# Optimization experiments

Hardware: AMD Instinct MI355X
Metric: run time of the kernel (lower is better)

The kernel has to match this reference:

```python
import jax, jax.numpy as jnp
import numpy as np
import math

B, S, D, H = 2, 2048, 1024, 16
HD = D // H  # head dim = 64


def setup_inputs() -> dict:
    key = jax.random.key(0)
    ks = jax.random.split(key, 8)
    scale = 1.0 / math.sqrt(D)
    return {
        "x": jax.random.normal(ks[0], (B, S, D), dtype=jnp.float32),
        "mask": jax.random.randint(ks[1], (B, S, S), 0, 2).astype(bool),
        "Wq": jax.random.normal(ks[2], (D, D), dtype=jnp.float32) * scale,
        "bq": jax.random.normal(ks[3], (D,), dtype=jnp.float32) * 0.01,
        "Wk": jax.random.normal(ks[4], (D, D), dtype=jnp.float32) * scale,
        "bk": jax.random.normal(ks[5], (D,), dtype=jnp.float32) * 0.01,
        "Wv": jax.random.normal(ks[6], (D, D), dtype=jnp.float32) * scale,
        "bv": jax.random.normal(ks[7], (D,), dtype=jnp.float32) * 0.01,
    }


def reference(x, mask, Wq, bq, Wk, bk, Wv, bv):
    # Linear projections (weights stored as [in, out])
    q = x @ Wq + bq  # [B,S,D]
    k = x @ Wk + bk
    v = x @ Wv + bv
    # split heads -> [B,H,S,HD]
    q = q.reshape(B, S, H, HD).transpose(0, 2, 1, 3)
    k = k.reshape(B, S, H, HD).transpose(0, 2, 1, 3)
    v = v.reshape(B, S, H, HD).transpose(0, 2, 1, 3)
    scores = jnp.einsum("bhqd,bhkd->bhqk", q, k) / jnp.sqrt(jnp.float32(HD))
    # Faithful to the source: masked_fill_(mask, -inf) is immediately
    # overwritten by masked_fill_(mask, 0), so masked positions end up 0
    # BEFORE the softmax (a quirk of the original module).
    scores = jnp.where(mask[:, None, :, :], 0.0, scores)
    attn = jax.nn.softmax(scores, axis=-1)  # dropout=0.0 (eval)
    out = jnp.einsum("bhqk,bhkd->bhqd", attn, v)
    return out.transpose(0, 2, 1, 3).reshape(B, S, D)
```

## Files before the change

### kernel.cpp

```cpp
#include <hip/hip_runtime.h>
#include <cstdint>
#include <cstddef>

static constexpr int B_ = 2, S_ = 2048, D_ = 1024, H_ = 16, HD_ = 64;

typedef float f32x4 __attribute__((ext_vector_type(4)));
typedef short bf16x8 __attribute__((ext_vector_type(8)));

__device__ __forceinline__ unsigned short f2bf(float f) {
    union { float f; unsigned int u; } v; v.f = f;
    unsigned int r = v.u + 0x7FFFu + ((v.u >> 16) & 1u);
    return (unsigned short)(r >> 16);
}

__device__ __forceinline__ unsigned pack2bf(float a, float b) {
#if __has_builtin(__builtin_amdgcn_cvt_pk_bf16_f32)
    auto p = __builtin_amdgcn_cvt_pk_bf16_f32(a, b);
    unsigned u; __builtin_memcpy(&u, &p, 4);
    return u;
#else
    return (unsigned)f2bf(a) | ((unsigned)f2bf(b) << 16);
#endif
}

__device__ __forceinline__ void gload_lds16(const void* g, void* l) {
    __builtin_amdgcn_global_load_lds(
        (const __attribute__((address_space(1))) void*)g,
        (__attribute__((address_space(3))) void*)l, 16, 0, 0);
}

__global__ __launch_bounds__(256)
void prep(const float* __restrict__ x, unsigned short* __restrict__ xo,
          const int* __restrict__ m, unsigned char* __restrict__ mo,
          const float* __restrict__ Wq, const float* __restrict__ Wk,
          const float* __restrict__ Wv, unsigned short* __restrict__ wt) {
    __shared__ unsigned short Ts[64][72];
    const int bid = blockIdx.x, t = threadIdx.x;
    if (bid < 2048) {
        size_t i = ((size_t)bid * 256 + t) * 8;
        float4 a = *(const float4*)(x + i);
        float4 c = *(const float4*)(x + i + 4);
        uint4 r;
        r.x = pack2bf(a.x, a.y); r.y = pack2bf(a.z, a.w);
        r.z = pack2bf(c.x, c.y); r.w = pack2bf(c.z, c.w);
        *(uint4*)(xo + i) = r;
    } else if (bid < 4096) {
        size_t i = ((size_t)(bid - 2048) * 256 + t) * 16;
        uint4 r;
        unsigned w[4];
        #pragma unroll
        for (int g = 0; g < 4; ++g) {
            int4 v = *(const int4*)(m + i + g * 4);
            w[g] = (v.x ? 1u : 0u) | (v.y ? 1u << 8 : 0u) |
                   (v.z ? 1u << 16 : 0u) | (v.w ? 1u << 24 : 0u);
        }
        r.x = w[0]; r.y = w[1]; r.z = w[2]; r.w = w[3];
        *(uint4*)(mo + i) = r;
    } else {
        const int tid = bid - 4096;
        const int mat = tid >> 8, tile = tid & 255;
        const float* __restrict__ W = (mat == 0) ? Wq : (mat == 1) ? Wk : Wv;
        unsigned short* __restrict__ o = wt + (size_t)mat * D_ * D_;
        const int n0 = (tile & 15) * 64, k0 = (tile >> 4) * 64;
        {
            const int nl = t & 63, kb = t >> 6;
            #pragma unroll
            for (int i = 0; i < 16; ++i) {
                int k = kb + i * 4;
                Ts[nl][k] = f2bf(W[(size_t)(k0 + k) * D_ + n0 + nl]);
            }
        }
        __syncthreads();
        {
            const int kl = t & 63, nb = t >> 6;
            #pragma unroll
            for (int i = 0; i < 16; ++i) {
                int n = nb + i * 4;
                o[(size_t)(n0 + n) * D_ + k0 + kl] = Ts[n][kl];
            }
        }
    }
}

__global__ __launch_bounds__(256)
void qkv_gemm(const unsigned short* __restrict__ xb, const unsigned short* __restrict__ wt,
              const float* __restrict__ bq, const float* __restrict__ bk,
              const float* __restrict__ bv,
              unsigned short* __restrict__ qo, unsigned short* __restrict__ ko,
              unsigned short* __restrict__ vto) {
    const int bx = blockIdx.x;
    const int by = blockIdx.y;
    const int mat = bx >> 3;
    const int ncol0 = (bx & 7) * 128;
    const float* __restrict__ bias = (mat == 0) ? bq : (mat == 1) ? bk : bv;
    const unsigned short* __restrict__ Wm = wt + (size_t)mat * D_ * D_;

    __shared__ unsigned short As[2][128 * 32];
    __shared__ unsigned short Bs[2][128 * 32];

    const int t = threadIdx.x;
    const int w = t >> 6, lane = t & 63;
    const int l15 = lane & 15, quad = lane >> 4;
    const int mw = (w >> 1) * 64, nw = (w & 1) * 64;
    const int rowBase = by * 128;

    const int r16 = lane >> 2;
    const int sslot = lane & 3;
    const int sg = (sslot ^ ((r16 >> 1) & 3)) * 8;
    const int rcol = (quad ^ ((l15 >> 1) & 3)) * 8;

    f32x4 acc[4][4] = {};

    #pragma unroll
    for (int j = 0; j < 2; ++j) {
        const int r0 = w * 32 + j * 16;
        gload_lds16(xb + (size_t)(rowBase + r0 + r16) * D_ + sg, &As[0][r0 * 32]);
        gload_lds16(Wm + (size_t)(ncol0 + r0 + r16) * D_ + sg, &Bs[0][r0 * 32]);
    }

    for (int it = 0; it < 32; ++it) {
        const int cur = it & 1;
        __syncthreads();
        if (it + 1 < 32) {
            const int ktn = (it + 1) * 32;
            #pragma unroll
            for (int j = 0; j < 2; ++j) {
                const int r0 = w * 32 + j * 16;
                gload_lds16(xb + (size_t)(rowBase + r0 + r16) * D_ + ktn + sg,
                            &As[cur ^ 1][r0 * 32]);
                gload_lds16(Wm + (size_t)(ncol0 + r0 + r16) * D_ + ktn + sg,
                            &Bs[cur ^ 1][r0 * 32]);
            }
        }

        bf16x8 a[4], b[4];
        #pragma unroll
        for (int i = 0; i < 4; ++i)
            a[i] = *(const bf16x8*)&As[cur][(mw + i * 16 + l15) * 32 + rcol];
        #pragma unroll
        for (int j = 0; j < 4; ++j)
            b[j] = *(const bf16x8*)&Bs[cur][(nw + j * 16 + l15) * 32 + rcol];
        #pragma unroll
        for (int i = 0; i < 4; ++i)
            #pragma unroll
            for (int j = 0; j < 4; ++j)
                acc[i][j] = __builtin_amdgcn_mfma_f32_16x16x32_bf16(a[i], b[j], acc[i][j], 0, 0, 0);
    }

    if (mat < 2) {
        unsigned short* __restrict__ O = (mat == 0) ? qo : ko;
        const float osc = (mat == 0) ? 0.18033688011112443f : 1.0f;
        #pragma unroll
        for (int j = 0; j < 4; ++j) {
            const int col = ncol0 + nw + j * 16 + l15;
            const float bb = bias[col];
            #pragma unroll
            for (int i = 0; i < 4; ++i)
                #pragma unroll
                for (int r = 0; r < 4; ++r) {
                    const int m = rowBase + mw + i * 16 + quad * 4 + r;
                    O[(size_t)m * D_ + col] = f2bf((acc[i][j][r] + bb) * osc);
                }
        }
    } else {
        #pragma unroll
        for (int j = 0; j < 4; ++j) {
            const int col = ncol0 + nw + j * 16 + l15;
            const float bb = bias[col];
            const int hh = col >> 6, hd = col & 63;
            #pragma unroll
            for (int i = 0; i < 4; ++i) {
                const int m0 = rowBase + mw + i * 16 + quad * 4;
                const int bg = m0 >> 11, s0 = m0 & 2047;
                ushort4 pk;
                pk.x = f2bf(acc[i][j][0] + bb);
                pk.y = f2bf(acc[i][j][1] + bb);
                pk.z = f2bf(acc[i][j][2] + bb);
                pk.w = f2bf(acc[i][j][3] + bb);
                *(ushort4*)&vto[(((size_t)bg * H_ + hh) * HD_ + hd) * S_ + s0] = pk;
            }
        }
    }
}

__global__ __launch_bounds__(256)
void attn_mfma(const unsigned short* __restrict__ qmat,
               const unsigned short* __restrict__ kmat,
               const unsigned short* __restrict__ vtg,
               const unsigned char* __restrict__ msk, float* __restrict__ out) {
    const int h = blockIdx.x, qt = blockIdx.y, b = blockIdx.z;
    const int t = threadIdx.x, w = t >> 6, lane = t & 63;
    const int l15 = lane & 15, quad = lane >> 4;
    const int q0 = qt * 128;

    __shared__ unsigned short Ks[2][64 * 64];
    __shared__ unsigned short Vs[2][64 * 64];
    __shared__ __align__(16) unsigned short Ps[128][72];

    const size_t bh = (size_t)b * S_ * D_ + (size_t)h * HD_;
    const unsigned short* __restrict__ qp = qmat + bh;
    const unsigned short* __restrict__ kp = kmat + bh;
    const unsigned short* __restrict__ vp = vtg + ((size_t)b * H_ + h) * HD_ * S_;
    const unsigned char* __restrict__ mb = msk + (size_t)b * S_ * S_;

    const int rs = lane >> 3, sslot = lane & 7;
    const int sg = (sslot ^ rs) * 8;

    bf16x8 qfr[2][2];
    #pragma unroll
    for (int nt = 0; nt < 2; ++nt)
        #pragma unroll
        for (int kst = 0; kst < 2; ++kst)
            qfr[nt][kst] = *(const bf16x8*)(qp +
                (size_t)(q0 + w * 32 + nt * 16 + l15) * D_ + kst * 32 + quad * 8);

    f32x4 accO[2][4] = {};
    f32x4 lsA[2] = {};
    bf16x8 ones;
    #pragma unroll
    for (int i = 0; i < 8; ++i) ones[i] = (short)0x3F80;

    #pragma unroll
    for (int j = 0; j < 2; ++j) {
        const int rb = w * 16 + j * 8;
        gload_lds16(kp + (size_t)(rb + rs) * D_ + sg, &Ks[0][rb * 64]);
        gload_lds16(vp + (size_t)(rb + rs) * S_ + sg, &Vs[0][rb * 64]);
    }

    for (int it = 0; it < 32; ++it) {
        const int cur = it & 1;
        const int kt = it * 64;
        __syncthreads();

        unsigned mu[2][4];
        #pragma unroll
        for (int nt = 0; nt < 2; ++nt) {
            const int qr = w * 32 + nt * 16 + l15;
            const unsigned char* __restrict__ mrow = mb + (size_t)(q0 + qr) * S_ + kt;
            #pragma unroll
            for (int mt = 0; mt < 4; ++mt)
                mu[nt][mt] = *(const unsigned*)(mrow + mt * 16 + quad * 4);
        }

        if (it + 1 < 32) {
            const int ktn = kt + 64;
            #pragma unroll
            for (int j = 0; j < 2; ++j) {
                const int rb = w * 16 + j * 8;
                gload_lds16(kp + (size_t)(ktn + rb + rs) * D_ + sg, &Ks[cur ^ 1][rb * 64]);
                gload_lds16(vp + (size_t)(rb + rs) * S_ + ktn + sg, &Vs[cur ^ 1][rb * 64]);
            }
        }

        f32x4 sc[4][2] = {};
        #pragma unroll
        for (int kst = 0; kst < 2; ++kst) {
            bf16x8 kfr[4];
            #pragma unroll
            for (int mt = 0; mt < 4; ++mt) {
                const int R = mt * 16 + l15;
                kfr[mt] = *(const bf16x8*)&Ks[cur][R * 64 + (((kst * 4 + quad) ^ (l15 & 7)) * 8)];
            }
            #pragma unroll
            for (int mt = 0; mt < 4; ++mt)
                #pragma unroll
                for (int nt = 0; nt < 2; ++nt)
                    sc[mt][nt] = __builtin_amdgcn_mfma_f32_16x16x32_bf16(kfr[mt], qfr[nt][kst], sc[mt][nt], 0, 0, 0);
        }

        #pragma unroll
        for (int nt = 0; nt < 2; ++nt) {
            const int qr = w * 32 + nt * 16 + l15;
            #pragma unroll
            for (int mt = 0; mt < 4; ++mt) {
                float p[4];
                #pragma unroll
                for (int r = 0; r < 4; ++r) {
                    float e = __builtin_amdgcn_exp2f(sc[mt][nt][r]);
                    p[r] = ((mu[nt][mt] >> (8 * r)) & 0xFFu) ? 1.0f : e;
                }
                uint2 pk;
                pk.x = pack2bf(p[0], p[1]);
                pk.y = pack2bf(p[2], p[3]);
                *(uint2*)&Ps[qr][mt * 16 + quad * 4] = pk;
            }
        }

        #pragma unroll
        for (int kst = 0; kst < 2; ++kst) {
            bf16x8 vfr[4];
            #pragma unroll
            for (int dt = 0; dt < 4; ++dt) {
                const int R = dt * 16 + l15;
                vfr[dt] = *(const bf16x8*)&Vs[cur][R * 64 + (((kst * 4 + quad) ^ (l15 & 7)) * 8)];
            }
            #pragma unroll
            for (int mt = 0; mt < 2; ++mt) {
                bf16x8 pfr = *(const bf16x8*)&Ps[w * 32 + mt * 16 + l15][kst * 32 + quad * 8];
                #pragma unroll
                for (int dt = 0; dt < 4; ++dt)
                    accO[mt][dt] = __builtin_amdgcn_mfma_f32_16x16x32_bf16(pfr, vfr[dt], accO[mt][dt], 0, 0, 0);
                lsA[mt] = __builtin_amdgcn_mfma_f32_16x16x32_bf16(pfr, ones, lsA[mt], 0, 0, 0);
            }
        }
    }

    float* __restrict__ ob = out + ((size_t)b * S_ + q0) * D_ + (size_t)h * HD_;
    #pragma unroll
    for (int mt = 0; mt < 2; ++mt)
        #pragma unroll
        for (int r = 0; r < 4; ++r) {
            const float inv = 1.0f / lsA[mt][r];
            const int qr = w * 32 + mt * 16 + quad * 4 + r;
            #pragma unroll
            for (int dt = 0; dt < 4; ++dt)
                ob[(size_t)qr * D_ + dt * 16 + l15] = accO[mt][dt][r] * inv;
        }
}

extern "C" void kernel_launch(void* const* d_in, const int* in_sizes, int n_in,
                              void* d_out, int out_size, void* d_ws, size_t ws_size,
                              hipStream_t stream) {
    (void)in_sizes; (void)n_in; (void)out_size; (void)ws_size;
    const float* x    = (const float*)d_in[0];
    const int*   mask = (const int*)d_in[1];
    const float* Wq   = (const float*)d_in[2];
    const float* bq   = (const float*)d_in[3];
    const float* Wk   = (const float*)d_in[4];
    const float* bk   = (const float*)d_in[5];
    const float* Wv   = (const float*)d_in[6];
    const float* bv   = (const float*)d_in[7];
    float* out = (float*)d_out;

    const size_t M1 = (size_t)1024 * 1024;
    unsigned short* xb  = (unsigned short*)d_ws;
    unsigned short* wtb = xb + 4 * M1;
    unsigned short* qb  = wtb + 3 * M1;
    unsigned short* kb  = qb + 4 * M1;
    unsigned short* vtb = kb + 4 * M1;
    unsigned char*  mk  = (unsigned char*)(vtb + 4 * M1);

    prep<<<4864, 256, 0, stream>>>(x, xb, mask, mk, Wq, Wk, Wv, wtb);
    qkv_gemm<<<dim3(24, 32), 256, 0, stream>>>(xb, wtb, bq, bk, bv, qb, kb, vtb);
    attn_mfma<<<dim3(16, 16, 2), 256, 0, stream>>>(qb, kb, vtb, mk, out);
}
```

Baseline: 234.7 us.

## Split attention over key halves with a combine pass, load V fragments from global

The attention kernel now splits the key range into two halves. This doubles the grid to 1024 blocks so more CUs are busy, and each half writes unnormalized partial outputs and row sums, with the first half's output stored in bf16. A new combine kernel adds the two partial outputs and normalizes by the summed row sums. V fragments are now read directly from global memory instead of being staged through LDS. The mask is stored inverted so that masking becomes a multiply by the mask byte before exp2, and the P tile in LDS gets an XOR swizzle. The trade-offs are an extra launch, extra traffic for the partial outputs, and some precision loss from the bf16 partial.

```diff
diff --git a/kernel.cpp b/kernel.cpp
--- a/kernel.cpp
+++ b/kernel.cpp
@@ -11,6 +11,10 @@
     union { float f; unsigned int u; } v; v.f = f;
     unsigned int r = v.u + 0x7FFFu + ((v.u >> 16) & 1u);
     return (unsigned short)(r >> 16);
+}
+__device__ __forceinline__ float bf2f(unsigned short h) {
+    union { unsigned int u; float f; } v; v.u = ((unsigned int)h) << 16;
+    return v.f;
 }
 
 __device__ __forceinline__ unsigned pack2bf(float a, float b) {
@@ -20,6 +24,19 @@
     return u;
 #else
     return (unsigned)f2bf(a) | ((unsigned)f2bf(b) << 16);
+#endif
+}
+
+__device__ __forceinline__ float ubyte2f(unsigned u, int r) {
+#if __has_builtin(__builtin_amdgcn_cvt_f32_ubyte0)
+    switch (r) {
+        case 0: return __builtin_amdgcn_cvt_f32_ubyte0(u);
+        case 1: return __builtin_amdgcn_cvt_f32_ubyte1(u);
+        case 2: return __builtin_amdgcn_cvt_f32_ubyte2(u);
+        default: return __builtin_amdgcn_cvt_f32_ubyte3(u);
+    }
+#else
+    return (float)((u >> (8 * r)) & 0xFFu);
 #endif
 }
 
@@ -51,8 +68,8 @@
         #pragma unroll
         for (int g = 0; g < 4; ++g) {
             int4 v = *(const int4*)(m + i + g * 4);
-            w[g] = (v.x ? 1u : 0u) | (v.y ? 1u << 8 : 0u) |
-                   (v.z ? 1u << 16 : 0u) | (v.w ? 1u << 24 : 0u);
+            w[g] = (v.x ? 0u : 1u) | (v.y ? 0u : 1u << 8) |
+                   (v.z ? 0u : 1u << 16) | (v.w ? 0u : 1u << 24);
         }
         r.x = w[0]; r.y = w[1]; r.z = w[2]; r.w = w[3];
         *(uint4*)(mo + i) = r;
@@ -187,15 +204,18 @@
 void attn_mfma(const unsigned short* __restrict__ qmat,
                const unsigned short* __restrict__ kmat,
                const unsigned short* __restrict__ vtg,
-               const unsigned char* __restrict__ msk, float* __restrict__ out) {
-    const int h = blockIdx.x, qt = blockIdx.y, b = blockIdx.z;
+               const unsigned char* __restrict__ msk,
+               unsigned short* __restrict__ O0, float* __restrict__ O1,
+               float* __restrict__ lws) {
+    const int qt = blockIdx.x, h = blockIdx.y;
+    const int b = blockIdx.z >> 1, half = blockIdx.z & 1;
     const int t = threadIdx.x, w = t >> 6, lane = t & 63;
     const int l15 = lane & 15, quad = lane >> 4;
     const int q0 = qt * 128;
+    const int kb0 = half * 1024;
 
     __shared__ unsigned short Ks[2][64 * 64];
-    __shared__ unsigned short Vs[2][64 * 64];
-    __shared__ __align__(16) unsigned short Ps[128][72];
+    __shared__ unsigned short Ps[128 * 64];
 
     const size_t bh = (size_t)b * S_ * D_ + (size_t)h * HD_;
     const unsigned short* __restrict__ qp = qmat + bh;
@@ -205,6 +225,7 @@
 
     const int rs = lane >> 3, sslot = lane & 7;
     const int sg = (sslot ^ rs) * 8;
+    const int l7 = l15 & 7;
 
     bf16x8 qfr[2][2];
     #pragma unroll
@@ -223,13 +244,12 @@
     #pragma unroll
     for (int j = 0; j < 2; ++j) {
         const int rb = w * 16 + j * 8;
-        gload_lds16(kp + (size_t)(rb + rs) * D_ + sg, &Ks[0][rb * 64]);
-        gload_lds16(vp + (size_t)(rb + rs) * S_ + sg, &Vs[0][rb * 64]);
-    }
-
-    for (int it = 0; it < 32; ++it) {
+        gload_lds16(kp + (size_t)(kb0 + rb + rs) * D_ + sg, &Ks[0][rb * 64]);
+    }
+
+    for (int it = 0; it < 16; ++it) {
         const int cur = it & 1;
-        const int kt = it * 64;
+        const int kt = kb0 + it * 64;
         __syncthreads();
 
         unsigned mu[2][4];
@@ -242,13 +262,12 @@
                 mu[nt][mt] = *(const unsigned*)(mrow + mt * 16 + quad * 4);
         }
 
-        if (it + 1 < 32) {
+        if (it + 1 < 16) {
             const int ktn = kt + 64;
             #pragma unroll
             for (int j = 0; j < 2; ++j) {
                 const int rb = w * 16 + j * 8;
                 gload_lds16(kp + (size_t)(ktn + rb + rs) * D_ + sg, &Ks[cur ^ 1][rb * 64]);
-                gload_lds16(vp + (size_t)(rb + rs) * S_ + ktn + sg, &Vs[cur ^ 1][rb * 64]);
             }
         }
 
@@ -259,7 +278,7 @@
             #pragma unroll
             for (int mt = 0; mt < 4; ++mt) {
                 const int R = mt * 16 + l15;
-                kfr[mt] = *(const bf16x8*)&Ks[cur][R * 64 + (((kst * 4 + quad) ^ (l15 & 7)) * 8)];
+                kfr[mt] = *(const bf16x8*)&Ks[cur][R * 64 + ((kst * 4 + quad) ^ l7) * 8];
             }
             #pragma unroll
             for (int mt = 0; mt < 4; ++mt)
@@ -276,13 +295,14 @@
                 float p[4];
                 #pragma unroll
                 for (int r = 0; r < 4; ++r) {
-                    float e = __builtin_amdgcn_exp2f(sc[mt][nt][r]);
-                    p[r] = ((mu[nt][mt] >> (8 * r)) & 0xFFu) ? 1.0f : e;
+                    float fm = ubyte2f(mu[nt][mt], r);
+                    p[r] = __builtin_amdgcn_exp2f(sc[mt][nt][r] * fm);
                 }
                 uint2 pk;
                 pk.x = pack2bf(p[0], p[1]);
                 pk.y = pack2bf(p[2], p[3]);
-                *(uint2*)&Ps[qr][mt * 16 + quad * 4] = pk;
+                const int gw = (mt * 2 + (quad >> 1)) ^ l7;
+                *(uint2*)&Ps[qr * 64 + gw * 8 + (quad & 1) * 4] = pk;
             }
         }
 
@@ -290,13 +310,12 @@
         for (int kst = 0; kst < 2; ++kst) {
             bf16x8 vfr[4];
             #pragma unroll
-            for (int dt = 0; dt < 4; ++dt) {
-                const int R = dt * 16 + l15;
-                vfr[dt] = *(const bf16x8*)&Vs[cur][R * 64 + (((kst * 4 + quad) ^ (l15 & 7)) * 8)];
-            }
+            for (int dt = 0; dt < 4; ++dt)
+                vfr[dt] = *(const bf16x8*)(vp + (size_t)(dt * 16 + l15) * S_ + kt + kst * 32 + quad * 8);
             #pragma unroll
             for (int mt = 0; mt < 2; ++mt) {
-                bf16x8 pfr = *(const bf16x8*)&Ps[w * 32 + mt * 16 + l15][kst * 32 + quad * 8];
+                const int R = w * 32 + mt * 16 + l15;
+                bf16x8 pfr = *(const bf16x8*)&Ps[R * 64 + ((kst * 4 + quad) ^ l7) * 8];
                 #pragma unroll
                 for (int dt = 0; dt < 4; ++dt)
                     accO[mt][dt] = __builtin_amdgcn_mfma_f32_16x16x32_bf16(pfr, vfr[dt], accO[mt][dt], 0, 0, 0);
@@ -305,17 +324,50 @@
         }
     }
 
-    float* __restrict__ ob = out + ((size_t)b * S_ + q0) * D_ + (size_t)h * HD_;
-    #pragma unroll
-    for (int mt = 0; mt < 2; ++mt)
-        #pragma unroll
-        for (int r = 0; r < 4; ++r) {
-            const float inv = 1.0f / lsA[mt][r];
-            const int qr = w * 32 + mt * 16 + quad * 4 + r;
-            #pragma unroll
-            for (int dt = 0; dt < 4; ++dt)
-                ob[(size_t)qr * D_ + dt * 16 + l15] = accO[mt][dt][r] * inv;
-        }
+    float* __restrict__ lp = lws + (((size_t)half * B_ + b) * H_ + h) * S_ + q0;
+    if (half == 0) {
+        unsigned short* __restrict__ ob = O0 + ((size_t)b * S_ + q0) * D_ + (size_t)h * HD_;
+        #pragma unroll
+        for (int mt = 0; mt < 2; ++mt)
+            #pragma unroll
+            for (int r = 0; r < 4; ++r) {
+                const int qr = w * 32 + mt * 16 + quad * 4 + r;
+                if (l15 == 0) lp[qr] = lsA[mt][r];
+                #pragma unroll
+                for (int dt = 0; dt < 4; ++dt)
+                    ob[(size_t)qr * D_ + dt * 16 + l15] = f2bf(accO[mt][dt][r]);
+            }
+    } else {
+        float* __restrict__ ob = O1 + ((size_t)b * S_ + q0) * D_ + (size_t)h * HD_;
+        #pragma unroll
+        for (int mt = 0; mt < 2; ++mt)
+            #pragma unroll
+            for (int r = 0; r < 4; ++r) {
+                const int qr = w * 32 + mt * 16 + quad * 4 + r;
+                if (l15 == 0) lp[qr] = lsA[mt][r];
+                #pragma unroll
+                for (int dt = 0; dt < 4; ++dt)
+                    ob[(size_t)qr * D_ + dt * 16 + l15] = accO[mt][dt][r];
+            }
+    }
+}
+
+__global__ __launch_bounds__(256)
+void combine(const unsigned short* __restrict__ O0, float* __restrict__ out,
+             const float* __restrict__ lws) {
+    const size_t i = ((size_t)blockIdx.x * 256 + threadIdx.x) * 4;
+    const int sf = (int)(i >> 10);
+    const int b = sf >> 11, s = sf & 2047;
+    const int h = ((int)i & 1023) >> 6;
+    const float l0 = lws[(((size_t)0 * B_ + b) * H_ + h) * S_ + s];
+    const float l1 = lws[(((size_t)1 * B_ + b) * H_ + h) * S_ + s];
+    const float inv = 1.0f / (l0 + l1);
+    ushort4 a = *(const ushort4*)(O0 + i);
+    float4 c = *(const float4*)(out + i);
+    float4 r;
+    r.x = (bf2f(a.x) + c.x) * inv; r.y = (bf2f(a.y) + c.y) * inv;
+    r.z = (bf2f(a.z) + c.z) * inv; r.w = (bf2f(a.w) + c.w) * inv;
+    *(float4*)(out + i) = r;
 }
 
 extern "C" void kernel_launch(void* const* d_in, const int* in_sizes, int n_in,
@@ -332,15 +384,19 @@
     const float* bv   = (const float*)d_in[7];
     float* out = (float*)d_out;
 
-    const size_t M1 = (size_t)1024 * 1024;
-    unsigned short* xb  = (unsigned short*)d_ws;
-    unsigned short* wtb = xb + 4 * M1;
-    unsigned short* qb  = wtb + 3 * M1;
-    unsigned short* kb  = qb + 4 * M1;
-    unsigned short* vtb = kb + 4 * M1;
-    unsigned char*  mk  = (unsigned char*)(vtb + 4 * M1);
+    const size_t MB = (size_t)1 << 20;
+    char* base = (char*)d_ws;
+    unsigned short* qb  = (unsigned short*)(base);
+    unsigned short* kb  = (unsigned short*)(base + 8 * MB);
+    unsigned short* vtb = (unsigned short*)(base + 16 * MB);
+    unsigned char*  mk  = (unsigned char*)(base + 24 * MB);
+    unsigned short* xb  = (unsigned short*)(base + 32 * MB);
+    unsigned short* wtb = (unsigned short*)(base + 40 * MB);
+    unsigned short* O0  = (unsigned short*)(base + 32 * MB);
+    float* lws = (float*)(base + 40 * MB);
 
     prep<<<4864, 256, 0, stream>>>(x, xb, mask, mk, Wq, Wk, Wv, wtb);
     qkv_gemm<<<dim3(24, 32), 256, 0, stream>>>(xb, wtb, bq, bk, bv, qb, kb, vtb);
-    attn_mfma<<<dim3(16, 16, 2), 256, 0, stream>>>(qb, kb, vtb, mk, out);
-}
+    attn_mfma<<<dim3(16, 16, 4), 256, 0, stream>>>(qb, kb, vtb, mk, O0, out, lws);
+    combine<<<4096, 256, 0, stream>>>(O0, out, lws);
+}
```

After: 297.2 us. 1.27x slower.
